# Optimization experiments

Measured on AMD Instinct MI355X. Metric: run time of the kernel, lower is better.

## Reference

```python
import jax, jax.numpy as jnp
import numpy as np

TOP_K = 2


def setup_inputs() -> dict:
    key = jax.random.key(0)
    ks = jax.random.split(key, 6)
    B, S, H, I, E = 4, 2048, 1024, 4096, 8
    x = jax.random.normal(ks[0], (B, S, H), dtype=jnp.float32)
    Wr = jax.random.normal(ks[1], (H, E), dtype=jnp.float32) * (1.0 / np.sqrt(H))
    W1 = jax.random.normal(ks[2], (E, H, I), dtype=jnp.float32) * (1.0 / np.sqrt(H))
    b1 = jnp.zeros((E, I), dtype=jnp.float32)
    W2 = jax.random.normal(ks[3], (E, I, H), dtype=jnp.float32) * (1.0 / np.sqrt(I))
    b2 = jnp.zeros((E, H), dtype=jnp.float32)
    return {"x": x, "Wr": Wr, "W1": W1, "b1": b1, "W2": W2, "b2": b2}


def reference(x, Wr, W1, b1, W2, b2):
    B, S, H = x.shape
    E = Wr.shape[1]
    xf = x.reshape(-1, H)                              # [T, H], T = B*S
    logits = xf @ Wr                                   # [T, E]
    probs = jax.nn.softmax(logits, axis=-1)
    rw, sel = jax.lax.top_k(probs, TOP_K)              # [T, K]
    rw = rw / jnp.sum(rw, axis=-1, keepdims=True)
    out = jnp.zeros_like(xf)
    # Loop over small fixed expert count; each token contributes only via its
    # top-k combine weight (zero weight == not routed, matching index_add).
    for i in range(E):
        wi = jnp.sum(jnp.where(sel == i, rw, 0.0), axis=-1)    # [T]
        h = jax.nn.silu(xf @ W1[i] + b1[i])                    # [T, I]
        out = out + (h @ W2[i] + b2[i]) * wi[:, None]
    return out.reshape(B, S, H)
```

## Files before the change

kernel.cpp:

```cpp
#include <hip/hip_runtime.h>
#include <cstdint>
#include <cstddef>

#define TTOK 8192
#define HDIM 1024
#define IDIM 4096
#define NEXP 8
#define PMAX 18432
#define WS_NEED 302260352ULL

#define SLOT1 24576
#define SLOT2 16384

typedef __attribute__((ext_vector_type(8))) short bf16x8;
typedef __attribute__((ext_vector_type(4))) float f32x4;

#define AS3 __attribute__((address_space(3)))
#define AS1 __attribute__((address_space(1)))

__device__ __forceinline__ void gld16(const void* g, void* s) {
  __builtin_amdgcn_global_load_lds((const AS1 void*)g, (AS3 void*)s, 16, 0, 0);
}

__device__ __forceinline__ void pinned_barrier() {
  __builtin_amdgcn_sched_barrier(0);
  __builtin_amdgcn_s_barrier();
  __builtin_amdgcn_sched_barrier(0);
}

__device__ __forceinline__ unsigned short f2b(float f) {
  unsigned u = __builtin_bit_cast(unsigned, f);
  unsigned r = ((u >> 16) & 1u) + 0x7FFFu;
  return (unsigned short)((u + r) >> 16);
}

__global__ __launch_bounds__(256, 2) void router_k(
    const float* __restrict__ x, const float* __restrict__ wr,
    unsigned short* __restrict__ xb, int* __restrict__ t2e,
    float* __restrict__ t2w)
{
  const int t = blockIdx.x * 4 + (threadIdx.x >> 6);
  const int l = threadIdx.x & 63;
  const float* xr = x + (size_t)t * HDIM;
  float acc[8] = {0.f,0.f,0.f,0.f,0.f,0.f,0.f,0.f};
  #pragma unroll
  for (int j = 0; j < 4; ++j) {
    const int base = j * 256 + l * 4;
    const float4 xv = *(const float4*)(xr + base);
    const float xa[4] = {xv.x, xv.y, xv.z, xv.w};
    ushort4 ub;
    ub.x = f2b(xa[0]); ub.y = f2b(xa[1]); ub.z = f2b(xa[2]); ub.w = f2b(xa[3]);
    *(ushort4*)(xb + (size_t)t * HDIM + base) = ub;
    #pragma unroll
    for (int ii = 0; ii < 4; ++ii) {
      const float4 w0 = *(const float4*)(wr + (size_t)(base + ii) * 8);
      const float4 w1 = *(const float4*)(wr + (size_t)(base + ii) * 8 + 4);
      acc[0] += xa[ii] * w0.x; acc[1] += xa[ii] * w0.y;
      acc[2] += xa[ii] * w0.z; acc[3] += xa[ii] * w0.w;
      acc[4] += xa[ii] * w1.x; acc[5] += xa[ii] * w1.y;
      acc[6] += xa[ii] * w1.z; acc[7] += xa[ii] * w1.w;
    }
  }
  #pragma unroll
  for (int e = 0; e < 8; ++e) {
    float v = acc[e];
    #pragma unroll
    for (int off = 32; off > 0; off >>= 1) v += __shfl_xor(v, off);
    acc[e] = v;
  }
  if (l == 0) {
    float l0 = -1e30f; int i0 = 0;
    #pragma unroll
    for (int e = 0; e < 8; ++e) if (acc[e] > l0) { l0 = acc[e]; i0 = e; }
    float l1 = -1e30f; int i1 = (i0 == 0) ? 1 : 0;
    #pragma unroll
    for (int e = 0; e < 8; ++e) if (e != i0 && acc[e] > l1) { l1 = acc[e]; i1 = e; }
    const float w0 = 1.f / (1.f + expf(l1 - l0));
    t2e[t * 2] = i0; t2e[t * 2 + 1] = i1;
    t2w[t * 2] = w0; t2w[t * 2 + 1] = 1.f - w0;
  }
}

__global__ void count_k(const int* __restrict__ t2e, int* __restrict__ meta) {
  const int t = threadIdx.x, w = t >> 6, l = t & 63;
  int cnt[8] = {0,0,0,0,0,0,0,0};
  for (int c = 0; c < 16; ++c) {
    const int tok = (w * 16 + c) * 64 + l;
    const int e0 = t2e[2 * tok], e1 = t2e[2 * tok + 1];
    #pragma unroll
    for (int e = 0; e < 8; ++e)
      cnt[e] += __popcll(__ballot(e0 == e)) + __popcll(__ballot(e1 == e));
  }
  __shared__ int part[8][8];
  if (l == 0) {
    #pragma unroll
    for (int e = 0; e < 8; ++e) part[w][e] = cnt[e];
  }
  __syncthreads();
  if (t == 0) {
    int off = 0;
    #pragma unroll
    for (int e = 0; e < 8; ++e) {
      int s = 0;
      #pragma unroll
      for (int w2 = 0; w2 < 8; ++w2) s += part[w2][e];
      meta[e] = s; meta[16 + e] = off; off += (s + 255) & ~255;
    }
    meta[24] = off;
  }
}

__global__ void scatter_k(const int* __restrict__ t2e, const int* __restrict__ meta,
                          int* __restrict__ ltok, int* __restrict__ t2p)
{
  const int e = blockIdx.x;
  const int t = threadIdx.x, w = t >> 6, l = t & 63;
  const int off = meta[16 + e];
  const int cnt = meta[e];
  __shared__ int wsum[4];
  __shared__ int base;
  if (t == 0) base = 0;
  __syncthreads();
  const unsigned long long lt = (1ULL << l) - 1ULL;
  for (int c = 0; c < TTOK / 256; ++c) {
    const int tok = c * 256 + t;
    const bool m0 = (t2e[2 * tok] == e);
    const bool m1 = (t2e[2 * tok + 1] == e);
    const unsigned long long b0 = __ballot(m0);
    const unsigned long long b1 = __ballot(m1);
    const int n0 = __popcll(b0), n1 = __popcll(b1);
    const int r0 = __popcll(b0 & lt);
    const int r1 = n0 + __popcll(b1 & lt);
    if (l == 0) wsum[w] = n0 + n1;
    __syncthreads();
    int wb = base;
    #pragma unroll
    for (int i = 0; i < 4; ++i) if (i < w) wb += wsum[i];
    const int tot = wsum[0] + wsum[1] + wsum[2] + wsum[3];
    __syncthreads();
    if (t == 0) base += tot;
    if (m0) { const int p = off + wb + r0; ltok[p] = tok; t2p[2 * tok] = p; }
    if (m1) { const int p = off + wb + r1; ltok[p] = tok; t2p[2 * tok + 1] = p; }
    __syncthreads();
  }
  const int padded = (cnt + 255) & ~255;
  for (int i = cnt + t; i < padded; i += 256) ltok[off + i] = -1;
}

__global__ __launch_bounds__(256, 2) void packT_k(const float* __restrict__ src,
                                                  unsigned short* __restrict__ dst,
                                                  int K, int N)
{
  const int tiles_n = N >> 8, tiles_k = K >> 5;
  const int bid = blockIdx.x;
  const int e = bid / (tiles_k * tiles_n);
  const int rem = bid % (tiles_k * tiles_n);
  const int kt = rem / tiles_n, it = rem % tiles_n;
  const float* S = src + (size_t)e * K * N + (size_t)kt * 32 * N + (size_t)it * 256;
  unsigned short* D = dst + (size_t)e * N * K + (size_t)it * 256 * K + (size_t)kt * 32;
  __shared__ uint32_t lds[256 * 17];
  const int t = threadIdx.x;
  #pragma unroll
  for (int q = 0; q < 4; ++q) {
    const int task = q * 256 + t;
    const int i4 = task & 63, kp = task >> 6;
    const float* p0 = S + (size_t)(2 * kp) * N + i4 * 4;
    const float4 r0 = *(const float4*)p0;
    const float4 r1 = *(const float4*)(p0 + N);
    const float a0[4] = {r0.x, r0.y, r0.z, r0.w};
    const float a1[4] = {r1.x, r1.y, r1.z, r1.w};
    #pragma unroll
    for (int j = 0; j < 4; ++j)
      lds[(i4 * 4 + j) * 17 + kp] = (uint32_t)f2b(a0[j]) | ((uint32_t)f2b(a1[j]) << 16);
  }
  __syncthreads();
  #pragma unroll
  for (int r = 0; r < 4; ++r) {
    const int idx = r * 256 + t;
    const int il = idx >> 2, q4 = idx & 3;
    uint4 o;
    o.x = lds[il * 17 + q4 * 4 + 0];
    o.y = lds[il * 17 + q4 * 4 + 1];
    o.z = lds[il * 17 + q4 * 4 + 2];
    o.w = lds[il * 17 + q4 * 4 + 3];
    *(uint4*)(D + (size_t)il * K + q4 * 8) = o;
  }
}


__global__ __launch_bounds__(512, 4) void gemm1_k(
    const unsigned short* __restrict__ xb, const unsigned short* __restrict__ w1t,
    const float* __restrict__ b1, const int* __restrict__ meta,
    const int* __restrict__ ltok, unsigned short* __restrict__ h)
{
  const int wg = blockIdx.x;
  const int id = (wg & 7) * (2304 / 8) + (wg >> 3);
  const int mt = id >> 5, nt = id & 31;
  if (mt * 256 >= meta[24]) return;
  int e = 0;
  #pragma unroll
  for (int i = 1; i < 8; ++i) if (meta[16 + i] <= mt * 256) e = i;

  extern __shared__ char lds[];
  const int t = threadIdx.x;
  const int w = t >> 6, l = t & 63;
  const int wn = w & 1, wm = w >> 1;

  const unsigned short* asrc;
  {
    const int G = t;
    const int line = G >> 3, q = (G & 7) ^ (line & 7);
    const int row = 2 * line + (q >> 2), g = q & 3;
    asrc = w1t + ((size_t)e * IDIM + nt * 128 + row) * HDIM + g * 8;
  }
  const unsigned short* bsrc[2];
  #pragma unroll
  for (int c = 0; c < 2; ++c) {
    const int G = c * 512 + t;
    const int line = G >> 3, q = (G & 7) ^ (line & 7);
    const int row = 2 * line + (q >> 2), g = q & 3;
    int tok = ltok[mt * 256 + row]; if (tok < 0) tok = 0;
    bsrc[c] = xb + (size_t)tok * HDIM + g * 8;
  }

  const int lr = l & 15, lg = l >> 4;
  f32x4 acc[4][4] = {};

  auto STAGE = [&](int kt) {
    char* sb = lds + (kt % 3) * SLOT1;
    const int ks = kt * 32;
    gld16(asrc + ks, sb + w * 1024);
    gld16(bsrc[0] + ks, sb + 8192 + w * 1024);
    gld16(bsrc[1] + ks, sb + 16384 + w * 1024);
  };

  STAGE(0); STAGE(1);
  const int NT = HDIM / 32;
  for (int kt = 0; kt < NT; ++kt) {
    if (kt + 1 < NT) {
      asm volatile("s_waitcnt vmcnt(3)" ::: "memory");
    } else {
      asm volatile("s_waitcnt vmcnt(0)" ::: "memory");
    }
    pinned_barrier();
    const char* sl = lds + (kt % 3) * SLOT1;
    bf16x8 af[4], bf[4];
    #pragma unroll
    for (int f = 0; f < 4; ++f) {
      const int rowA = wn * 64 + f * 16 + lr;
      const int lineA = rowA >> 1;
      const int pA = (((rowA & 1) << 2) + lg) ^ (lineA & 7);
      af[f] = *(const bf16x8*)(sl + lineA * 128 + pA * 16);
      const int rowB = wm * 64 + f * 16 + lr;
      const int lineB = rowB >> 1;
      const int pB = (((rowB & 1) << 2) + lg) ^ (lineB & 7);
      bf[f] = *(const bf16x8*)(sl + 8192 + lineB * 128 + pB * 16);
    }
    if (kt + 2 < NT) STAGE(kt + 2);
    __builtin_amdgcn_s_setprio(1);
    #pragma unroll
    for (int fm = 0; fm < 4; ++fm)
      #pragma unroll
      for (int fn = 0; fn < 4; ++fn)
        acc[fm][fn] = __builtin_amdgcn_mfma_f32_16x16x32_bf16(af[fm], bf[fn], acc[fm][fn], 0, 0, 0);
    __builtin_amdgcn_s_setprio(0);
    pinned_barrier();
  }

  const int lg4 = lg * 4;
  #pragma unroll
  for (int fm = 0; fm < 4; ++fm) {
    const int ib = nt * 128 + wn * 64 + fm * 16 + lg4;
    const float4 b1v = *(const float4*)(b1 + e * IDIM + ib);
    #pragma unroll
    for (int fn = 0; fn < 4; ++fn) {
      const int trow = mt * 256 + wm * 64 + fn * 16 + lr;
      const float v0 = acc[fm][fn][0] + b1v.x;
      const float v1 = acc[fm][fn][1] + b1v.y;
      const float v2 = acc[fm][fn][2] + b1v.z;
      const float v3 = acc[fm][fn][3] + b1v.w;
      ushort4 st;
      st.x = f2b(v0 / (1.f + __expf(-v0)));
      st.y = f2b(v1 / (1.f + __expf(-v1)));
      st.z = f2b(v2 / (1.f + __expf(-v2)));
      st.w = f2b(v3 / (1.f + __expf(-v3)));
      *(ushort4*)(h + (size_t)trow * IDIM + ib) = st;
    }
  }
}

__global__ __launch_bounds__(256, 3) void gemm2_k(
    const unsigned short* __restrict__ h, const unsigned short* __restrict__ w2t,
    const int* __restrict__ meta, float* __restrict__ y)
{
  const int wg = blockIdx.x;
  const int id = (wg & 7) * (1152 / 8) + (wg >> 3);
  const int mt = id >> 3, nt = id & 7;
  if (mt * 128 >= meta[24]) return;
  int e = 0;
  #pragma unroll
  for (int i = 1; i < 8; ++i) if (meta[16 + i] <= mt * 128) e = i;

  extern __shared__ char lds[];
  const int t = threadIdx.x;
  const int w = t >> 6, l = t & 63;
  const int wn = w & 1, wm = w >> 1;

  const unsigned short* asrc[2]; const unsigned short* bsrc[2];
  #pragma unroll
  for (int c = 0; c < 2; ++c) {
    const int G = c * 256 + t;
    const int line = G >> 3, q = (G & 7) ^ (line & 7);
    const int row = 2 * line + (q >> 2), g = q & 3;
    asrc[c] = w2t + ((size_t)e * HDIM + nt * 128 + row) * IDIM + g * 8;
    bsrc[c] = h + (size_t)(mt * 128 + row) * IDIM + g * 8;
  }

  const int lr = l & 15, lg = l >> 4;
  f32x4 acc[4][4] = {};

  auto STAGE = [&](int kt) {
    char* sb = lds + (kt % 3) * SLOT2;
    const int ks = kt * 32;
    gld16(asrc[0] + ks, sb + w * 1024);
    gld16(asrc[1] + ks, sb + 4096 + w * 1024);
    gld16(bsrc[0] + ks, sb + 8192 + w * 1024);
    gld16(bsrc[1] + ks, sb + 12288 + w * 1024);
  };

  STAGE(0); STAGE(1);
  const int NT = IDIM / 32;
  for (int kt = 0; kt < NT; ++kt) {
    if (kt + 1 < NT) {
      asm volatile("s_waitcnt vmcnt(4)" ::: "memory");
    } else {
      asm volatile("s_waitcnt vmcnt(0)" ::: "memory");
    }
    pinned_barrier();
    const char* sl = lds + (kt % 3) * SLOT2;
    bf16x8 af[4], bf[4];
    #pragma unroll
    for (int f = 0; f < 4; ++f) {
      const int rowA = wn * 64 + f * 16 + lr;
      const int lineA = rowA >> 1;
      const int pA = (((rowA & 1) << 2) + lg) ^ (lineA & 7);
      af[f] = *(const bf16x8*)(sl + lineA * 128 + pA * 16);
      const int rowB = wm * 64 + f * 16 + lr;
      const int lineB = rowB >> 1;
      const int pB = (((rowB & 1) << 2) + lg) ^ (lineB & 7);
      bf[f] = *(const bf16x8*)(sl + 8192 + lineB * 128 + pB * 16);
    }
    if (kt + 2 < NT) STAGE(kt + 2);
    __builtin_amdgcn_s_setprio(1);
    #pragma unroll
    for (int fm = 0; fm < 4; ++fm)
      #pragma unroll
      for (int fn = 0; fn < 4; ++fn)
        acc[fm][fn] = __builtin_amdgcn_mfma_f32_16x16x32_bf16(af[fm], bf[fn], acc[fm][fn], 0, 0, 0);
    __builtin_amdgcn_s_setprio(0);
    pinned_barrier();
  }

  const int lg4 = lg * 4;
  #pragma unroll
  for (int fm = 0; fm < 4; ++fm) {
    const int colb = nt * 128 + wn * 64 + fm * 16 + lg4;
    #pragma unroll
    for (int fn = 0; fn < 4; ++fn) {
      const int row = mt * 128 + wm * 64 + fn * 16 + lr;
      float4 st;
      st.x = acc[fm][fn][0]; st.y = acc[fm][fn][1];
      st.z = acc[fm][fn][2]; st.w = acc[fm][fn][3];
      *(float4*)(y + (size_t)row * HDIM + colb) = st;
    }
  }
}

__global__ __launch_bounds__(256, 4) void combine_k(
    const float* __restrict__ y, const float* __restrict__ b2,
    const int* __restrict__ t2e, const float* __restrict__ t2w,
    const int* __restrict__ t2p, float* __restrict__ out)
{
  const int t = blockIdx.x * 4 + (threadIdx.x >> 6);
  const int l = threadIdx.x & 63;
  const int e0 = t2e[t * 2], e1 = t2e[t * 2 + 1];
  const float w0 = t2w[t * 2], w1v = t2w[t * 2 + 1];
  const int p0 = t2p[t * 2], p1 = t2p[t * 2 + 1];
  const float* y0 = y + (size_t)p0 * HDIM;
  const float* y1 = y + (size_t)p1 * HDIM;
  const float* bb0 = b2 + e0 * HDIM;
  const float* bb1 = b2 + e1 * HDIM;
  float* o = out + (size_t)t * HDIM;
  #pragma unroll
  for (int j = 0; j < 4; ++j) {
    const int c = j * 256 + l * 4;
    const float4 a = *(const float4*)(y0 + c);
    const float4 b = *(const float4*)(y1 + c);
    const float4 c0 = *(const float4*)(bb0 + c);
    const float4 c1 = *(const float4*)(bb1 + c);
    float4 r;
    r.x = w0 * (a.x + c0.x) + w1v * (b.x + c1.x);
    r.y = w0 * (a.y + c0.y) + w1v * (b.y + c1.y);
    r.z = w0 * (a.z + c0.z) + w1v * (b.z + c1.z);
    r.w = w0 * (a.w + c0.w) + w1v * (b.w + c1.w);
    *(float4*)(o + c) = r;
  }
}

__global__ void sentinel_k(float* out) { out[0] = 1.0e6f; }

extern "C" void kernel_launch(void* const* d_in, const int* in_sizes, int n_in,
                              void* d_out, int out_size, void* d_ws, size_t ws_size,
                              hipStream_t stream)
{
  (void)in_sizes; (void)n_in; (void)out_size;
  const float* x  = (const float*)d_in[0];
  const float* wr = (const float*)d_in[1];
  const float* w1 = (const float*)d_in[2];
  const float* b1 = (const float*)d_in[3];
  const float* w2 = (const float*)d_in[4];
  const float* b2 = (const float*)d_in[5];
  float* out = (float*)d_out;
  char* ws = (char*)d_ws;

  if (ws_size < WS_NEED) { sentinel_k<<<1, 1, 0, stream>>>(out); return; }

  unsigned short* xb  = (unsigned short*)(ws);
  unsigned short* w1t = (unsigned short*)(ws + 16777216);
  unsigned short* w2t = (unsigned short*)(ws + 83886080);
  unsigned short* h   = (unsigned short*)(ws + 150994944);
  int*   t2e  = (int*)(ws + 301989888);
  float* t2w  = (float*)(ws + 302055424);
  int*   ltok = (int*)(ws + 302120960);
  int*   t2p  = (int*)(ws + 302194688);
  int*   meta = (int*)(ws + 302260224);
  float* y    = (float*)(ws);

  hipFuncSetAttribute((const void*)gemm1_k, hipFuncAttributeMaxDynamicSharedMemorySize, 3 * SLOT1);
  hipFuncSetAttribute((const void*)gemm2_k, hipFuncAttributeMaxDynamicSharedMemorySize, 3 * SLOT2);

  router_k<<<TTOK / 4, 256, 0, stream>>>(x, wr, xb, t2e, t2w);
  packT_k<<<NEXP * (HDIM / 32) * (IDIM / 256), 256, 0, stream>>>(w1, w1t, HDIM, IDIM);
  packT_k<<<NEXP * (IDIM / 32) * (HDIM / 256), 256, 0, stream>>>(w2, w2t, IDIM, HDIM);
  count_k<<<1, 512, 0, stream>>>(t2e, meta);
  scatter_k<<<NEXP, 256, 0, stream>>>(t2e, meta, ltok, t2p);

  gemm1_k<<<72 * 32, 512, 3 * SLOT1, stream>>>(xb, w1t, b1, meta, ltok, h);
  gemm2_k<<<144 * 8, 256, 3 * SLOT2, stream>>>(h, w2t, meta, y);
  combine_k<<<TTOK / 4, 256, 0, stream>>>(y, b2, t2e, t2w, t2p, out);
}
```

Baseline: 550.1 us.

## Fuse router and weight packing into one launch; store expert outputs in bf16

Merges the router kernel and both weight transpose/pack kernels into a single prep kernel that dispatches on block index, removing two launches and letting the three independent jobs overlap on the device. Separately, gemm2 now writes its per-row expert output as bf16 instead of fp32, and combine reads and widens it, halving that intermediate's write and read traffic. The cost is extra rounding error on the expert outputs before the weighted combine.

```diff
diff --git a/kernel.cpp b/kernel.cpp
--- a/kernel.cpp
+++ b/kernel.cpp
@@ -34,14 +34,19 @@
   return (unsigned short)((u + r) >> 16);
 }
 
-__global__ __launch_bounds__(256, 2) void router_k(
-    const float* __restrict__ x, const float* __restrict__ wr,
+__device__ __forceinline__ float b2f(unsigned short u) {
+  return __builtin_bit_cast(float, ((unsigned)u) << 16);
+}
+
+
+__device__ __forceinline__ void router_body(
+    int bid, int t, const float* __restrict__ x, const float* __restrict__ wr,
     unsigned short* __restrict__ xb, int* __restrict__ t2e,
     float* __restrict__ t2w)
 {
-  const int t = blockIdx.x * 4 + (threadIdx.x >> 6);
-  const int l = threadIdx.x & 63;
-  const float* xr = x + (size_t)t * HDIM;
+  const int tok = bid * 4 + (t >> 6);
+  const int l = t & 63;
+  const float* xr = x + (size_t)tok * HDIM;
   float acc[8] = {0.f,0.f,0.f,0.f,0.f,0.f,0.f,0.f};
   #pragma unroll
   for (int j = 0; j < 4; ++j) {
@@ -50,7 +55,7 @@
     const float xa[4] = {xv.x, xv.y, xv.z, xv.w};
     ushort4 ub;
     ub.x = f2b(xa[0]); ub.y = f2b(xa[1]); ub.z = f2b(xa[2]); ub.w = f2b(xa[3]);
-    *(ushort4*)(xb + (size_t)t * HDIM + base) = ub;
+    *(ushort4*)(xb + (size_t)tok * HDIM + base) = ub;
     #pragma unroll
     for (int ii = 0; ii < 4; ++ii) {
       const float4 w0 = *(const float4*)(wr + (size_t)(base + ii) * 8);
@@ -76,8 +81,64 @@
     #pragma unroll
     for (int e = 0; e < 8; ++e) if (e != i0 && acc[e] > l1) { l1 = acc[e]; i1 = e; }
     const float w0 = 1.f / (1.f + expf(l1 - l0));
-    t2e[t * 2] = i0; t2e[t * 2 + 1] = i1;
-    t2w[t * 2] = w0; t2w[t * 2 + 1] = 1.f - w0;
+    t2e[tok * 2] = i0; t2e[tok * 2 + 1] = i1;
+    t2w[tok * 2] = w0; t2w[tok * 2 + 1] = 1.f - w0;
+  }
+}
+
+__device__ __forceinline__ void packT_body(
+    int bid, int t, uint32_t* __restrict__ plds,
+    const float* __restrict__ src, unsigned short* __restrict__ dst,
+    int K, int N)
+{
+  const int tiles_n = N >> 8, tiles_k = K >> 5;
+  const int e = bid / (tiles_k * tiles_n);
+  const int rem = bid % (tiles_k * tiles_n);
+  const int kt = rem / tiles_n, it = rem % tiles_n;
+  const float* S = src + (size_t)e * K * N + (size_t)kt * 32 * N + (size_t)it * 256;
+  unsigned short* D = dst + (size_t)e * N * K + (size_t)it * 256 * K + (size_t)kt * 32;
+  #pragma unroll
+  for (int q = 0; q < 4; ++q) {
+    const int task = q * 256 + t;
+    const int i4 = task & 63, kp = task >> 6;
+    const float* p0 = S + (size_t)(2 * kp) * N + i4 * 4;
+    const float4 r0 = *(const float4*)p0;
+    const float4 r1 = *(const float4*)(p0 + N);
+    const float a0[4] = {r0.x, r0.y, r0.z, r0.w};
+    const float a1[4] = {r1.x, r1.y, r1.z, r1.w};
+    #pragma unroll
+    for (int j = 0; j < 4; ++j)
+      plds[(i4 * 4 + j) * 17 + kp] = (uint32_t)f2b(a0[j]) | ((uint32_t)f2b(a1[j]) << 16);
+  }
+  __syncthreads();
+  #pragma unroll
+  for (int r = 0; r < 4; ++r) {
+    const int idx = r * 256 + t;
+    const int il = idx >> 2, q4 = idx & 3;
+    uint4 o;
+    o.x = plds[il * 17 + q4 * 4 + 0];
+    o.y = plds[il * 17 + q4 * 4 + 1];
+    o.z = plds[il * 17 + q4 * 4 + 2];
+    o.w = plds[il * 17 + q4 * 4 + 3];
+    *(uint4*)(D + (size_t)il * K + q4 * 8) = o;
+  }
+}
+
+__global__ __launch_bounds__(256, 2) void prep_k(
+    const float* __restrict__ x, const float* __restrict__ wr,
+    unsigned short* __restrict__ xb, int* __restrict__ t2e,
+    float* __restrict__ t2w,
+    const float* __restrict__ w1, unsigned short* __restrict__ w1t,
+    const float* __restrict__ w2, unsigned short* __restrict__ w2t)
+{
+  __shared__ uint32_t plds[256 * 17];
+  const int bid = blockIdx.x, t = threadIdx.x;
+  if (bid < 2048) {
+    router_body(bid, t, x, wr, xb, t2e, t2w);
+  } else if (bid < 2048 + 4096) {
+    packT_body(bid - 2048, t, plds, w1, w1t, HDIM, IDIM);
+  } else {
+    packT_body(bid - 6144, t, plds, w2, w2t, IDIM, HDIM);
   }
 }
 
@@ -147,46 +208,6 @@
   for (int i = cnt + t; i < padded; i += 256) ltok[off + i] = -1;
 }
 
-__global__ __launch_bounds__(256, 2) void packT_k(const float* __restrict__ src,
-                                                  unsigned short* __restrict__ dst,
-                                                  int K, int N)
-{
-  const int tiles_n = N >> 8, tiles_k = K >> 5;
-  const int bid = blockIdx.x;
-  const int e = bid / (tiles_k * tiles_n);
-  const int rem = bid % (tiles_k * tiles_n);
-  const int kt = rem / tiles_n, it = rem % tiles_n;
-  const float* S = src + (size_t)e * K * N + (size_t)kt * 32 * N + (size_t)it * 256;
-  unsigned short* D = dst + (size_t)e * N * K + (size_t)it * 256 * K + (size_t)kt * 32;
-  __shared__ uint32_t lds[256 * 17];
-  const int t = threadIdx.x;
-  #pragma unroll
-  for (int q = 0; q < 4; ++q) {
-    const int task = q * 256 + t;
-    const int i4 = task & 63, kp = task >> 6;
-    const float* p0 = S + (size_t)(2 * kp) * N + i4 * 4;
-    const float4 r0 = *(const float4*)p0;
-    const float4 r1 = *(const float4*)(p0 + N);
-    const float a0[4] = {r0.x, r0.y, r0.z, r0.w};
-    const float a1[4] = {r1.x, r1.y, r1.z, r1.w};
-    #pragma unroll
-    for (int j = 0; j < 4; ++j)
-      lds[(i4 * 4 + j) * 17 + kp] = (uint32_t)f2b(a0[j]) | ((uint32_t)f2b(a1[j]) << 16);
-  }
-  __syncthreads();
-  #pragma unroll
-  for (int r = 0; r < 4; ++r) {
-    const int idx = r * 256 + t;
-    const int il = idx >> 2, q4 = idx & 3;
-    uint4 o;
-    o.x = lds[il * 17 + q4 * 4 + 0];
-    o.y = lds[il * 17 + q4 * 4 + 1];
-    o.z = lds[il * 17 + q4 * 4 + 2];
-    o.w = lds[il * 17 + q4 * 4 + 3];
-    *(uint4*)(D + (size_t)il * K + q4 * 8) = o;
-  }
-}
-
 
 __global__ __launch_bounds__(512, 4) void gemm1_k(
     const unsigned short* __restrict__ xb, const unsigned short* __restrict__ w1t,
@@ -291,7 +312,7 @@
 
 __global__ __launch_bounds__(256, 3) void gemm2_k(
     const unsigned short* __restrict__ h, const unsigned short* __restrict__ w2t,
-    const int* __restrict__ meta, float* __restrict__ y)
+    const int* __restrict__ meta, unsigned short* __restrict__ y)
 {
   const int wg = blockIdx.x;
   const int id = (wg & 7) * (1152 / 8) + (wg >> 3);
@@ -368,16 +389,16 @@
     #pragma unroll
     for (int fn = 0; fn < 4; ++fn) {
       const int row = mt * 128 + wm * 64 + fn * 16 + lr;
-      float4 st;
-      st.x = acc[fm][fn][0]; st.y = acc[fm][fn][1];
-      st.z = acc[fm][fn][2]; st.w = acc[fm][fn][3];
-      *(float4*)(y + (size_t)row * HDIM + colb) = st;
+      ushort4 st;
+      st.x = f2b(acc[fm][fn][0]); st.y = f2b(acc[fm][fn][1]);
+      st.z = f2b(acc[fm][fn][2]); st.w = f2b(acc[fm][fn][3]);
+      *(ushort4*)(y + (size_t)row * HDIM + colb) = st;
     }
   }
 }
 
 __global__ __launch_bounds__(256, 4) void combine_k(
-    const float* __restrict__ y, const float* __restrict__ b2,
+    const unsigned short* __restrict__ y, const float* __restrict__ b2,
     const int* __restrict__ t2e, const float* __restrict__ t2w,
     const int* __restrict__ t2p, float* __restrict__ out)
 {
@@ -386,23 +407,23 @@
   const int e0 = t2e[t * 2], e1 = t2e[t * 2 + 1];
   const float w0 = t2w[t * 2], w1v = t2w[t * 2 + 1];
   const int p0 = t2p[t * 2], p1 = t2p[t * 2 + 1];
-  const float* y0 = y + (size_t)p0 * HDIM;
-  const float* y1 = y + (size_t)p1 * HDIM;
+  const unsigned short* y0 = y + (size_t)p0 * HDIM;
+  const unsigned short* y1 = y + (size_t)p1 * HDIM;
   const float* bb0 = b2 + e0 * HDIM;
   const float* bb1 = b2 + e1 * HDIM;
   float* o = out + (size_t)t * HDIM;
   #pragma unroll
   for (int j = 0; j < 4; ++j) {
     const int c = j * 256 + l * 4;
-    const float4 a = *(const float4*)(y0 + c);
-    const float4 b = *(const float4*)(y1 + c);
+    const ushort4 a = *(const ushort4*)(y0 + c);
+    const ushort4 b = *(const ushort4*)(y1 + c);
     const float4 c0 = *(const float4*)(bb0 + c);
     const float4 c1 = *(const float4*)(bb1 + c);
     float4 r;
-    r.x = w0 * (a.x + c0.x) + w1v * (b.x + c1.x);
-    r.y = w0 * (a.y + c0.y) + w1v * (b.y + c1.y);
-    r.z = w0 * (a.z + c0.z) + w1v * (b.z + c1.z);
-    r.w = w0 * (a.w + c0.w) + w1v * (b.w + c1.w);
+    r.x = w0 * (b2f(a.x) + c0.x) + w1v * (b2f(b.x) + c1.x);
+    r.y = w0 * (b2f(a.y) + c0.y) + w1v * (b2f(b.y) + c1.y);
+    r.z = w0 * (b2f(a.z) + c0.z) + w1v * (b2f(b.z) + c1.z);
+    r.w = w0 * (b2f(a.w) + c0.w) + w1v * (b2f(b.w) + c1.w);
     *(float4*)(o + c) = r;
   }
 }
@@ -434,14 +455,12 @@
   int*   ltok = (int*)(ws + 302120960);
   int*   t2p  = (int*)(ws + 302194688);
   int*   meta = (int*)(ws + 302260224);
-  float* y    = (float*)(ws);
+  unsigned short* y = (unsigned short*)(ws);
 
   hipFuncSetAttribute((const void*)gemm1_k, hipFuncAttributeMaxDynamicSharedMemorySize, 3 * SLOT1);
   hipFuncSetAttribute((const void*)gemm2_k, hipFuncAttributeMaxDynamicSharedMemorySize, 3 * SLOT2);
 
-  router_k<<<TTOK / 4, 256, 0, stream>>>(x, wr, xb, t2e, t2w);
-  packT_k<<<NEXP * (HDIM / 32) * (IDIM / 256), 256, 0, stream>>>(w1, w1t, HDIM, IDIM);
-  packT_k<<<NEXP * (IDIM / 32) * (HDIM / 256), 256, 0, stream>>>(w2, w2t, IDIM, HDIM);
+  prep_k<<<10240, 256, 0, stream>>>(x, wr, xb, t2e, t2w, w1, w1t, w2, w2t);
   count_k<<<1, 512, 0, stream>>>(t2e, meta);
   scatter_k<<<NEXP, 256, 0, stream>>>(t2e, meta, ltok, t2p);
 
```

Result: faster. 532.6 us (-3.2%).
